# Kernel tuning notes

Measured on AMD Instinct MI355X. Metric: run time of the kernel, lower is better.

Reference implementation:

```python
import jax, jax.numpy as jnp
import numpy as np

N_EMBED = 1024
N_HEAD = 64  # head (value) dimension, per source: Linear(n_embed, n_head)
B = 8
C = 2048


def setup_inputs() -> dict:
    key = jax.random.key(0)
    k1, k2, k3, k4, k5 = jax.random.split(key, 5)
    bound = 1.0 / np.sqrt(N_EMBED)  # torch Linear default init range
    x = jax.random.normal(k1, (B, C, N_EMBED), dtype=jnp.float32)
    Wq = jax.random.uniform(k2, (N_EMBED, N_HEAD), dtype=jnp.float32, minval=-bound, maxval=bound)
    Wk = jax.random.uniform(k3, (N_EMBED, N_HEAD), dtype=jnp.float32, minval=-bound, maxval=bound)
    Wv = jax.random.uniform(k4, (N_EMBED, N_HEAD), dtype=jnp.float32, minval=-bound, maxval=bound)
    zero_mask = jax.random.randint(k5, (B, C), 0, 2) == 1
    return {"x": x, "Wq": Wq, "Wk": Wk, "Wv": Wv, "zero_mask": zero_mask}


def reference(x, Wq, Wk, Wv, zero_mask):
    # x: [B, C, n_embed]; zero_mask: [B, C] bool (zeroes whole query rows post-softmax)
    Bc, Cc, _ = x.shape
    q = x @ Wq  # [B, C, H]
    k = x @ Wk
    v = x @ Wv
    # NOTE: source scales by C**-0.5 (sequence length), not head_dim**-0.5
    scores = jnp.einsum('bqh,bkh->bqk', q, k) * (float(Cc) ** -0.5)  # [B, C, C]
    causal = jnp.tril(jnp.ones((Cc, Cc), dtype=bool))
    scores = jnp.where(causal[None], scores, -jnp.inf)
    a = jax.nn.softmax(scores, axis=-1)
    a = jnp.where(zero_mask[..., None], jnp.zeros((), dtype=a.dtype), a)  # post-softmax zero mask
    return a @ v  # [B, C, H]
```

## Files before the change

### kernel.cpp

```cpp
#include <hip/hip_runtime.h>
#include <math.h>


#define B_ 8
#define C_ 2048
#define E_ 1024
#define H_ 64
#define SCALE 0.02209708691207961f

typedef __attribute__((ext_vector_type(8))) short short8;
typedef __attribute__((ext_vector_type(4))) float floatx4;

union BF8 { short8 s8; unsigned int u[4]; };

static __device__ __forceinline__ unsigned int pack_bf2(float lo, float hi) {
    unsigned int a = __builtin_bit_cast(unsigned int, lo);
    unsigned int b = __builtin_bit_cast(unsigned int, hi);
    return (a >> 16) | (b & 0xFFFF0000u);
}
static __device__ __forceinline__ unsigned short f2bf(float f) {
    return (unsigned short)(__builtin_bit_cast(unsigned int, f) >> 16);
}
static __device__ __forceinline__ void load_lds16(const void* g, void* l) {
    __builtin_amdgcn_global_load_lds(
        (const __attribute__((address_space(1))) void*)g,
        (__attribute__((address_space(3))) void*)l, 16, 0, 0);
}

__global__ __launch_bounds__(256) void wcvt_kernel(
    const float* __restrict__ Wq, const float* __restrict__ Wk,
    const float* __restrict__ Wv, unsigned short* __restrict__ wt)
{
    __shared__ float lds[64][68];
    const int bid = (int)blockIdx.x;
    const int m = bid >> 4, kt = bid & 15, k0 = kt * 64;
    const float* W = (m == 0) ? Wq : (m == 1) ? Wk : Wv;
    const int t = (int)threadIdx.x;
#pragma unroll
    for (int j = 0; j < 4; j++) {
        int idx4 = j * 256 + t;
        int row = idx4 >> 4, c4 = idx4 & 15;
        float4 v = *(const float4*)(W + (size_t)(k0 + row) * 64 + c4 * 4);
        *(float4*)&lds[row][c4 * 4] = v;
    }
    __syncthreads();
#pragma unroll
    for (int j = 0; j < 2; j++) {
        int g = j * 256 + t;
        int n = g >> 3, kk = (g & 7) * 8;
        unsigned int o[4];
#pragma unroll
        for (int i = 0; i < 4; i++)
            o[i] = pack_bf2(lds[kk + 2 * i][n], lds[kk + 2 * i + 1][n]);
        *(uint4*)(wt + (size_t)(m * 64 + n) * 1024 + k0 + kk) =
            make_uint4(o[0], o[1], o[2], o[3]);
    }
}

__global__ __launch_bounds__(256, 2) void qkv_kernel(
    const float* __restrict__ X, const unsigned short* __restrict__ wt,
    unsigned short* __restrict__ qg, unsigned short* __restrict__ kg,
    unsigned short* __restrict__ vtile)
{
    __shared__ unsigned short wlds[2][192 * 64];
    __shared__ unsigned short vstage[64 * 40];

    const int t = (int)threadIdx.x;
    const int w = t >> 6, lane = t & 63;
    const int l15 = lane & 15, quad = lane >> 4;
    const int r0 = (int)blockIdx.x * 32;
    const int mrow = r0 + (w >> 1) * 16 + l15;
    const int ncol0 = (w & 1) * 96;

    const int srow_off = lane >> 3;
    const int sgs = lane & 7;

    floatx4 acc[6];
#pragma unroll
    for (int j = 0; j < 6; j++) acc[j] = (floatx4){0.f, 0.f, 0.f, 0.f};

#pragma unroll
    for (int j = 0; j < 6; j++) {
        const int region = w * 6 + j;
        const int row = region * 8 + srow_off;
        const int gsrc = sgs ^ (row & 7);
        load_lds16(wt + (size_t)row * 1024 + gsrc * 8, &wlds[0][region * 512]);
    }
    float4 xr[4];
#pragma unroll
    for (int kc = 0; kc < 2; kc++) {
        const float* xp = X + (size_t)mrow * E_ + kc * 32 + quad * 8;
        xr[kc * 2]     = *(const float4*)xp;
        xr[kc * 2 + 1] = *(const float4*)(xp + 4);
    }

    int buf = 0;
    for (int c = 0; c < 16; c++) {
        __syncthreads();
        float4 xr2[4];
        if (c < 15) {
            const int k0n = (c + 1) * 64;
#pragma unroll
            for (int kc = 0; kc < 2; kc++) {
                const float* xp = X + (size_t)mrow * E_ + k0n + kc * 32 + quad * 8;
                xr2[kc * 2]     = *(const float4*)xp;
                xr2[kc * 2 + 1] = *(const float4*)(xp + 4);
            }
#pragma unroll
            for (int j = 0; j < 6; j++) {
                const int region = w * 6 + j;
                const int row = region * 8 + srow_off;
                const int gsrc = sgs ^ (row & 7);
                load_lds16(wt + (size_t)row * 1024 + k0n + gsrc * 8,
                           &wlds[buf ^ 1][region * 512]);
            }
        }
#pragma unroll
        for (int kc = 0; kc < 2; kc++) {
            BF8 a;
            float4 f0 = xr[kc * 2], f1 = xr[kc * 2 + 1];
            a.u[0] = pack_bf2(f0.x, f0.y);
            a.u[1] = pack_bf2(f0.z, f0.w);
            a.u[2] = pack_bf2(f1.x, f1.y);
            a.u[3] = pack_bf2(f1.z, f1.w);
#pragma unroll
            for (int nt = 0; nt < 6; nt++) {
                const int n = ncol0 + nt * 16 + l15;
                const int g = kc * 4 + quad;
                short8 bfr = *(const short8*)&wlds[buf][n * 64 + (g ^ (n & 7)) * 8];
                acc[nt] = __builtin_amdgcn_mfma_f32_16x16x32_bf16(
                    a.s8, bfr, acc[nt], 0, 0, 0);
            }
        }
#pragma unroll
        for (int j = 0; j < 4; j++) xr[j] = xr2[j];
        buf ^= 1;
    }

    const int bb = r0 >> 11;
    const int keybase = r0 & 2047;
    const int rowl0 = (w >> 1) * 16 + quad * 4;
#pragma unroll
    for (int nt = 0; nt < 6; nt++) {
        const int n = ncol0 + nt * 16 + l15;
        if (n < 64) {
#pragma unroll
            for (int r = 0; r < 4; r++)
                qg[(size_t)(r0 + rowl0 + r) * 64 + n] = f2bf(acc[nt][r] * SCALE);
        } else if (n < 128) {
#pragma unroll
            for (int r = 0; r < 4; r++)
                kg[(size_t)(r0 + rowl0 + r) * 64 + (n - 64)] = f2bf(acc[nt][r]);
        } else {
            const int h = n - 128;
            unsigned int p0 = pack_bf2(acc[nt][0], acc[nt][1]);
            unsigned int p1 = pack_bf2(acc[nt][2], acc[nt][3]);
            *(unsigned int*)&vstage[h * 40 + rowl0] = p0;
            *(unsigned int*)&vstage[h * 40 + rowl0 + 2] = p1;
        }
    }
    __syncthreads();
    {
        const int h = t >> 2, part = t & 3;
        uint4 v = *(const uint4*)&vstage[h * 40 + part * 8];
        *(uint4*)(vtile + ((size_t)(bb * 32 + (keybase >> 6)) * 64 + h) * 64
                  + (keybase & 63) + part * 8) = v;
    }
}

__global__ __launch_bounds__(128, 2) void attn_kernel(
    const unsigned short* __restrict__ qg, const unsigned short* __restrict__ kg,
    const unsigned short* __restrict__ vtile, const int* __restrict__ zmask,
    float* __restrict__ opart, float* __restrict__ lpart,
    float* __restrict__ out)
{
    __shared__ unsigned short Klds[2][64 * 64];
    __shared__ unsigned short Vlds[2][64 * 64];
    __shared__ unsigned short Ps[2 * 16 * 88];

    const int t = (int)threadIdx.x;
    const int w = t >> 6, lane = t & 63;
    const int l15 = lane & 15, quad = lane >> 4;
    const int b = (int)blockIdx.x;
    const int qt = (int)blockIdx.y;
    const int z = (int)blockIdx.z;
    const int q0 = qt * 32;
    const int nkt = (q0 >> 6) + 1;
    const int t0 = z * 16;
    const int t1 = (z == 0) ? ((nkt < 16) ? nkt : 16) : nkt;
    if (t0 >= t1) return;

    const int qlo = q0 + w * 16;
    const int myrow = qlo + quad * 4;
    const int srow_off = lane >> 3, sgs = lane & 7;

    short8 qfr[2];
#pragma unroll
    for (int kc = 0; kc < 2; kc++)
        qfr[kc] = *(const short8*)(qg + ((size_t)b * C_ + qlo + l15) * 64
                                   + kc * 32 + quad * 8);

    floatx4 accO[4];
#pragma unroll
    for (int i = 0; i < 4; i++) accO[i] = (floatx4){0.f, 0.f, 0.f, 0.f};
    float lsum[4] = {0.f, 0.f, 0.f, 0.f};

#pragma unroll
    for (int j = 0; j < 4; j++) {
        const int region = w * 4 + j;
        const int row = region * 8 + srow_off;
        const int gsrc = sgs ^ (row & 7);
        load_lds16(kg + ((size_t)b * C_ + t0 * 64 + row) * 64 + gsrc * 8,
                   &Klds[0][region * 512]);
        load_lds16(vtile + (((size_t)b * 32 + t0) * 64 + row) * 64 + gsrc * 8,
                   &Vlds[0][region * 512]);
    }

    int buf = 0;
    for (int kt = t0; kt < t1; kt++) {
        __syncthreads();
        if (kt + 1 < t1) {
            const int k0n = (kt + 1) * 64;
#pragma unroll
            for (int j = 0; j < 4; j++) {
                const int region = w * 4 + j;
                const int row = region * 8 + srow_off;
                const int gsrc = sgs ^ (row & 7);
                load_lds16(kg + ((size_t)b * C_ + k0n + row) * 64 + gsrc * 8,
                           &Klds[buf ^ 1][region * 512]);
                load_lds16(vtile + (((size_t)b * 32 + kt + 1) * 64 + row) * 64 + gsrc * 8,
                           &Vlds[buf ^ 1][region * 512]);
            }
        }

        floatx4 s[4];
#pragma unroll
        for (int nt = 0; nt < 4; nt++) {
            const int row = nt * 16 + l15;
            short8 kf0 = *(const short8*)&Klds[buf][row * 64 + ((quad) ^ (row & 7)) * 8];
            short8 kf1 = *(const short8*)&Klds[buf][row * 64 + ((4 + quad) ^ (row & 7)) * 8];
            floatx4 zz = (floatx4){0.f, 0.f, 0.f, 0.f};
            zz = __builtin_amdgcn_mfma_f32_16x16x32_bf16(qfr[0], kf0, zz, 0, 0, 0);
            s[nt] = __builtin_amdgcn_mfma_f32_16x16x32_bf16(qfr[1], kf1, zz, 0, 0, 0);
        }
        float pr[4][4];
#pragma unroll
        for (int nt = 0; nt < 4; nt++)
#pragma unroll
            for (int r = 0; r < 4; r++) pr[nt][r] = __expf(s[nt][r]);
        if (kt == nkt - 1) {
            const int k0 = kt * 64;
#pragma unroll
            for (int nt = 0; nt < 4; nt++) {
                const int key = k0 + nt * 16 + l15;
#pragma unroll
                for (int r = 0; r < 4; r++)
                    if (key > myrow + r) pr[nt][r] = 0.f;
            }
        }
#pragma unroll
        for (int nt = 0; nt < 4; nt++)
#pragma unroll
            for (int r = 0; r < 4; r++) {
                lsum[r] += pr[nt][r];
                Ps[(w * 16 + quad * 4 + r) * 88 + nt * 16 + l15] = f2bf(pr[nt][r]);
            }
#pragma unroll
        for (int kc = 0; kc < 2; kc++) {
            short8 af = *(const short8*)&Ps[(w * 16 + l15) * 88 + kc * 32 + quad * 8];
#pragma unroll
            for (int nt = 0; nt < 4; nt++) {
                const int row = nt * 16 + l15;
                short8 vf = *(const short8*)&Vlds[buf][row * 64
                                + ((kc * 4 + quad) ^ (row & 7)) * 8];
                accO[nt] = __builtin_amdgcn_mfma_f32_16x16x32_bf16(
                    af, vf, accO[nt], 0, 0, 0);
            }
        }
        buf ^= 1;
    }

#pragma unroll
    for (int r = 0; r < 4; r++) {
        float v = lsum[r];
        v += __shfl_xor(v, 1);
        v += __shfl_xor(v, 2);
        v += __shfl_xor(v, 4);
        v += __shfl_xor(v, 8);
        lsum[r] = v;
    }

    if (q0 < 1024) {
        float inv[4];
#pragma unroll
        for (int r = 0; r < 4; r++) {
            int zm = zmask[b * C_ + myrow + r];
            inv[r] = zm ? 0.f : 1.0f / lsum[r];
        }
#pragma unroll
        for (int nt = 0; nt < 4; nt++)
#pragma unroll
            for (int r = 0; r < 4; r++)
                out[(size_t)(b * C_ + myrow + r) * 64 + nt * 16 + l15] =
                    accO[nt][r] * inv[r];
    } else {
        const int lrow = myrow - 1024;
        float* ob = opart + ((size_t)(z * 8 + b) * 1024 + lrow) * 64;
#pragma unroll
        for (int nt = 0; nt < 4; nt++)
#pragma unroll
            for (int r = 0; r < 4; r++)
                ob[(size_t)r * 64 + nt * 16 + l15] = accO[nt][r];
        if (l15 == 0) {
#pragma unroll
            for (int r = 0; r < 4; r++)
                lpart[(size_t)(z * 8 + b) * 1024 + lrow + r] = lsum[r];
        }
    }
}

__global__ __launch_bounds__(256) void combine_kernel(
    const float* __restrict__ opart, const float* __restrict__ lpart,
    const int* __restrict__ zmask, float* __restrict__ out)
{
    const int gid = (int)blockIdx.x * 256 + (int)threadIdx.x;
    const int b = gid >> 14;
    const int rem = gid & 16383;
    const int lrow = rem >> 4;
    const int f4 = rem & 15;

    const size_t o0 = ((size_t)(0 * 8 + b) * 1024 + lrow) * 64 + f4 * 4;
    const size_t o1 = ((size_t)(1 * 8 + b) * 1024 + lrow) * 64 + f4 * 4;
    float4 a = *(const float4*)(opart + o0);
    float4 c = *(const float4*)(opart + o1);
    float l = lpart[(size_t)(0 * 8 + b) * 1024 + lrow]
            + lpart[(size_t)(1 * 8 + b) * 1024 + lrow];
    const int row = 1024 + lrow;
    const float inv = zmask[b * C_ + row] ? 0.f : 1.0f / l;
    *(float4*)(out + (size_t)(b * C_ + row) * 64 + f4 * 4) =
        make_float4((a.x + c.x) * inv, (a.y + c.y) * inv,
                    (a.z + c.z) * inv, (a.w + c.w) * inv);
}

extern "C" void kernel_launch(void* const* d_in, const int* in_sizes, int n_in,
                              void* d_out, int out_size, void* d_ws, size_t ws_size,
                              hipStream_t stream) {
    const float* X  = (const float*)d_in[0];
    const float* Wq = (const float*)d_in[1];
    const float* Wk = (const float*)d_in[2];
    const float* Wv = (const float*)d_in[3];
    const int*   zm = (const int*)d_in[4];
    float* out = (float*)d_out;

    unsigned short* qg    = (unsigned short*)d_ws;
    unsigned short* kg    = qg    + (size_t)B_ * C_ * H_;
    unsigned short* vtile = kg    + (size_t)B_ * C_ * H_;
    unsigned short* wt    = vtile + (size_t)B_ * C_ * H_;
    float* opart = (float*)(wt + (size_t)192 * 1024);
    float* lpart = opart + (size_t)2 * 8 * 1024 * 64;

    wcvt_kernel<<<dim3(48), dim3(256), 0, stream>>>(Wq, Wk, Wv, wt);
    qkv_kernel<<<dim3(512), dim3(256), 0, stream>>>(X, wt, qg, kg, vtile);
    attn_kernel<<<dim3(B_, 64, 2), dim3(128), 0, stream>>>(
        qg, kg, vtile, zm, opart, lpart, out);
    combine_kernel<<<dim3(512), dim3(256), 0, stream>>>(opart, lpart, zm, out);
}
```

Measured before the change: 148.0 us.

## Drop LDS staging and shrink attention blocks to single-wave with finer KV split

```diff
diff --git a/kernel.cpp b/kernel.cpp
--- a/kernel.cpp
+++ b/kernel.cpp
@@ -20,11 +20,6 @@
 }
 static __device__ __forceinline__ unsigned short f2bf(float f) {
     return (unsigned short)(__builtin_bit_cast(unsigned int, f) >> 16);
-}
-static __device__ __forceinline__ void load_lds16(const void* g, void* l) {
-    __builtin_amdgcn_global_load_lds(
-        (const __attribute__((address_space(1))) void*)g,
-        (__attribute__((address_space(3))) void*)l, 16, 0, 0);
 }
 
 __global__ __launch_bounds__(256) void wcvt_kernel(
@@ -57,12 +52,11 @@
     }
 }
 
-__global__ __launch_bounds__(256, 2) void qkv_kernel(
+__global__ __launch_bounds__(256, 4) void qkv_kernel(
     const float* __restrict__ X, const unsigned short* __restrict__ wt,
     unsigned short* __restrict__ qg, unsigned short* __restrict__ kg,
     unsigned short* __restrict__ vtile)
 {
-    __shared__ unsigned short wlds[2][192 * 64];
     __shared__ unsigned short vstage[64 * 40];
 
     const int t = (int)threadIdx.x;
@@ -72,20 +66,10 @@
     const int mrow = r0 + (w >> 1) * 16 + l15;
     const int ncol0 = (w & 1) * 96;
 
-    const int srow_off = lane >> 3;
-    const int sgs = lane & 7;
-
     floatx4 acc[6];
 #pragma unroll
     for (int j = 0; j < 6; j++) acc[j] = (floatx4){0.f, 0.f, 0.f, 0.f};
 
-#pragma unroll
-    for (int j = 0; j < 6; j++) {
-        const int region = w * 6 + j;
-        const int row = region * 8 + srow_off;
-        const int gsrc = sgs ^ (row & 7);
-        load_lds16(wt + (size_t)row * 1024 + gsrc * 8, &wlds[0][region * 512]);
-    }
     float4 xr[4];
 #pragma unroll
     for (int kc = 0; kc < 2; kc++) {
@@ -94,25 +78,25 @@
         xr[kc * 2 + 1] = *(const float4*)(xp + 4);
     }
 
-    int buf = 0;
     for (int c = 0; c < 16; c++) {
-        __syncthreads();
+        const int k0 = c * 64;
+        short8 bfr[2][6];
+#pragma unroll
+        for (int kc = 0; kc < 2; kc++)
+#pragma unroll
+            for (int nt = 0; nt < 6; nt++) {
+                const int n = ncol0 + nt * 16 + l15;
+                bfr[kc][nt] = *(const short8*)(wt + (size_t)n * 1024 + k0
+                                              + kc * 32 + quad * 8);
+            }
         float4 xr2[4];
         if (c < 15) {
-            const int k0n = (c + 1) * 64;
+            const int k0n = k0 + 64;
 #pragma unroll
             for (int kc = 0; kc < 2; kc++) {
                 const float* xp = X + (size_t)mrow * E_ + k0n + kc * 32 + quad * 8;
                 xr2[kc * 2]     = *(const float4*)xp;
                 xr2[kc * 2 + 1] = *(const float4*)(xp + 4);
-            }
-#pragma unroll
-            for (int j = 0; j < 6; j++) {
-                const int region = w * 6 + j;
-                const int row = region * 8 + srow_off;
-                const int gsrc = sgs ^ (row & 7);
-                load_lds16(wt + (size_t)row * 1024 + k0n + gsrc * 8,
-                           &wlds[buf ^ 1][region * 512]);
             }
         }
 #pragma unroll
@@ -124,17 +108,12 @@
             a.u[2] = pack_bf2(f1.x, f1.y);
             a.u[3] = pack_bf2(f1.z, f1.w);
 #pragma unroll
-            for (int nt = 0; nt < 6; nt++) {
-                const int n = ncol0 + nt * 16 + l15;
-                const int g = kc * 4 + quad;
-                short8 bfr = *(const short8*)&wlds[buf][n * 64 + (g ^ (n & 7)) * 8];
+            for (int nt = 0; nt < 6; nt++)
                 acc[nt] = __builtin_amdgcn_mfma_f32_16x16x32_bf16(
-                    a.s8, bfr, acc[nt], 0, 0, 0);
-            }
+                    a.s8, bfr[kc][nt], acc[nt], 0, 0, 0);
         }
 #pragma unroll
         for (int j = 0; j < 4; j++) xr[j] = xr2[j];
-        buf ^= 1;
     }
 
     const int bb = r0 >> 11;
@@ -168,36 +147,31 @@
     }
 }
 
-__global__ __launch_bounds__(128, 2) void attn_kernel(
+__global__ __launch_bounds__(64, 4) void attn_kernel(
     const unsigned short* __restrict__ qg, const unsigned short* __restrict__ kg,
     const unsigned short* __restrict__ vtile, const int* __restrict__ zmask,
     float* __restrict__ opart, float* __restrict__ lpart,
     float* __restrict__ out)
 {
-    __shared__ unsigned short Klds[2][64 * 64];
-    __shared__ unsigned short Vlds[2][64 * 64];
-    __shared__ unsigned short Ps[2 * 16 * 88];
-
-    const int t = (int)threadIdx.x;
-    const int w = t >> 6, lane = t & 63;
+    __shared__ unsigned short Ps[16 * 88];
+
+    const int lane = (int)threadIdx.x;
     const int l15 = lane & 15, quad = lane >> 4;
     const int b = (int)blockIdx.x;
     const int qt = (int)blockIdx.y;
     const int z = (int)blockIdx.z;
-    const int q0 = qt * 32;
-    const int nkt = (q0 >> 6) + 1;
-    const int t0 = z * 16;
-    const int t1 = (z == 0) ? ((nkt < 16) ? nkt : 16) : nkt;
+    const int q0 = qt * 16;
+    const int nkt = (qt >> 2) + 1;
+    const int t0 = z * 8;
+    const int t1 = (t0 + 8 < nkt) ? (t0 + 8) : nkt;
     if (t0 >= t1) return;
-
-    const int qlo = q0 + w * 16;
-    const int myrow = qlo + quad * 4;
-    const int srow_off = lane >> 3, sgs = lane & 7;
+    const int ns = (nkt + 7) >> 3;
+    const int myrow = q0 + quad * 4;
 
     short8 qfr[2];
 #pragma unroll
     for (int kc = 0; kc < 2; kc++)
-        qfr[kc] = *(const short8*)(qg + ((size_t)b * C_ + qlo + l15) * 64
+        qfr[kc] = *(const short8*)(qg + ((size_t)b * C_ + q0 + l15) * 64
                                    + kc * 32 + quad * 8);
 
     floatx4 accO[4];
@@ -205,43 +179,31 @@
     for (int i = 0; i < 4; i++) accO[i] = (floatx4){0.f, 0.f, 0.f, 0.f};
     float lsum[4] = {0.f, 0.f, 0.f, 0.f};
 
-#pragma unroll
-    for (int j = 0; j < 4; j++) {
-        const int region = w * 4 + j;
-        const int row = region * 8 + srow_off;
-        const int gsrc = sgs ^ (row & 7);
-        load_lds16(kg + ((size_t)b * C_ + t0 * 64 + row) * 64 + gsrc * 8,
-                   &Klds[0][region * 512]);
-        load_lds16(vtile + (((size_t)b * 32 + t0) * 64 + row) * 64 + gsrc * 8,
-                   &Vlds[0][region * 512]);
-    }
-
-    int buf = 0;
     for (int kt = t0; kt < t1; kt++) {
-        __syncthreads();
-        if (kt + 1 < t1) {
-            const int k0n = (kt + 1) * 64;
-#pragma unroll
-            for (int j = 0; j < 4; j++) {
-                const int region = w * 4 + j;
-                const int row = region * 8 + srow_off;
-                const int gsrc = sgs ^ (row & 7);
-                load_lds16(kg + ((size_t)b * C_ + k0n + row) * 64 + gsrc * 8,
-                           &Klds[buf ^ 1][region * 512]);
-                load_lds16(vtile + (((size_t)b * 32 + kt + 1) * 64 + row) * 64 + gsrc * 8,
-                           &Vlds[buf ^ 1][region * 512]);
-            }
-        }
+        const int k0 = kt * 64;
+        short8 kf[4][2];
+#pragma unroll
+        for (int nt = 0; nt < 4; nt++)
+#pragma unroll
+            for (int kc = 0; kc < 2; kc++)
+                kf[nt][kc] = *(const short8*)(kg
+                    + ((size_t)b * C_ + k0 + nt * 16 + l15) * 64
+                    + kc * 32 + quad * 8);
+        short8 vf[4][2];
+#pragma unroll
+        for (int nt = 0; nt < 4; nt++)
+#pragma unroll
+            for (int kc = 0; kc < 2; kc++)
+                vf[nt][kc] = *(const short8*)(vtile
+                    + (((size_t)b * 32 + kt) * 64 + nt * 16 + l15) * 64
+                    + kc * 32 + quad * 8);
 
         floatx4 s[4];
 #pragma unroll
         for (int nt = 0; nt < 4; nt++) {
-            const int row = nt * 16 + l15;
-            short8 kf0 = *(const short8*)&Klds[buf][row * 64 + ((quad) ^ (row & 7)) * 8];
-            short8 kf1 = *(const short8*)&Klds[buf][row * 64 + ((4 + quad) ^ (row & 7)) * 8];
             floatx4 zz = (floatx4){0.f, 0.f, 0.f, 0.f};
-            zz = __builtin_amdgcn_mfma_f32_16x16x32_bf16(qfr[0], kf0, zz, 0, 0, 0);
-            s[nt] = __builtin_amdgcn_mfma_f32_16x16x32_bf16(qfr[1], kf1, zz, 0, 0, 0);
+            zz = __builtin_amdgcn_mfma_f32_16x16x32_bf16(qfr[0], kf[nt][0], zz, 0, 0, 0);
+            s[nt] = __builtin_amdgcn_mfma_f32_16x16x32_bf16(qfr[1], kf[nt][1], zz, 0, 0, 0);
         }
         float pr[4][4];
 #pragma unroll
@@ -249,7 +211,6 @@
 #pragma unroll
             for (int r = 0; r < 4; r++) pr[nt][r] = __expf(s[nt][r]);
         if (kt == nkt - 1) {
-            const int k0 = kt * 64;
 #pragma unroll
             for (int nt = 0; nt < 4; nt++) {
                 const int key = k0 + nt * 16 + l15;
@@ -263,21 +224,16 @@
 #pragma unroll
             for (int r = 0; r < 4; r++) {
                 lsum[r] += pr[nt][r];
-                Ps[(w * 16 + quad * 4 + r) * 88 + nt * 16 + l15] = f2bf(pr[nt][r]);
+                Ps[(quad * 4 + r) * 88 + nt * 16 + l15] = f2bf(pr[nt][r]);
             }
 #pragma unroll
         for (int kc = 0; kc < 2; kc++) {
-            short8 af = *(const short8*)&Ps[(w * 16 + l15) * 88 + kc * 32 + quad * 8];
-#pragma unroll
-            for (int nt = 0; nt < 4; nt++) {
-                const int row = nt * 16 + l15;
-                short8 vf = *(const short8*)&Vlds[buf][row * 64
-                                + ((kc * 4 + quad) ^ (row & 7)) * 8];
+            short8 af = *(const short8*)&Ps[l15 * 88 + kc * 32 + quad * 8];
+#pragma unroll
+            for (int nt = 0; nt < 4; nt++)
                 accO[nt] = __builtin_amdgcn_mfma_f32_16x16x32_bf16(
-                    af, vf, accO[nt], 0, 0, 0);
-            }
-        }
-        buf ^= 1;
+                    af, vf[nt][kc], accO[nt], 0, 0, 0);
+        }
     }
 
 #pragma unroll
@@ -290,7 +246,7 @@
         lsum[r] = v;
     }
 
-    if (q0 < 1024) {
+    if (ns == 1) {
         float inv[4];
 #pragma unroll
         for (int r = 0; r < 4; r++) {
@@ -304,8 +260,8 @@
                 out[(size_t)(b * C_ + myrow + r) * 64 + nt * 16 + l15] =
                     accO[nt][r] * inv[r];
     } else {
-        const int lrow = myrow - 1024;
-        float* ob = opart + ((size_t)(z * 8 + b) * 1024 + lrow) * 64;
+        const int lrow = myrow - 512;
+        float* ob = opart + ((size_t)(z * 8 + b) * 1536 + lrow) * 64;
 #pragma unroll
         for (int nt = 0; nt < 4; nt++)
 #pragma unroll
@@ -314,7 +270,7 @@
         if (l15 == 0) {
 #pragma unroll
             for (int r = 0; r < 4; r++)
-                lpart[(size_t)(z * 8 + b) * 1024 + lrow + r] = lsum[r];
+                lpart[(size_t)(z * 8 + b) * 1536 + lrow + r] = lsum[r];
         }
     }
 }
@@ -323,23 +279,25 @@
     const float* __restrict__ opart, const float* __restrict__ lpart,
     const int* __restrict__ zmask, float* __restrict__ out)
 {
+    const int b = (int)blockIdx.y;
     const int gid = (int)blockIdx.x * 256 + (int)threadIdx.x;
-    const int b = gid >> 14;
-    const int rem = gid & 16383;
-    const int lrow = rem >> 4;
-    const int f4 = rem & 15;
-
-    const size_t o0 = ((size_t)(0 * 8 + b) * 1024 + lrow) * 64 + f4 * 4;
-    const size_t o1 = ((size_t)(1 * 8 + b) * 1024 + lrow) * 64 + f4 * 4;
-    float4 a = *(const float4*)(opart + o0);
-    float4 c = *(const float4*)(opart + o1);
-    float l = lpart[(size_t)(0 * 8 + b) * 1024 + lrow]
-            + lpart[(size_t)(1 * 8 + b) * 1024 + lrow];
-    const int row = 1024 + lrow;
+    const int lrow = gid >> 4;
+    const int f4 = gid & 15;
+    const int row = 512 + lrow;
+    const int nkt = (row >> 6) + 1;
+    const int ns = (nkt + 7) >> 3;
+
+    float4 o = make_float4(0.f, 0.f, 0.f, 0.f);
+    float l = 0.f;
+    for (int zc = 0; zc < ns; zc++) {
+        float4 p = *(const float4*)(opart
+            + ((size_t)(zc * 8 + b) * 1536 + lrow) * 64 + f4 * 4);
+        o.x += p.x; o.y += p.y; o.z += p.z; o.w += p.w;
+        l += lpart[(size_t)(zc * 8 + b) * 1536 + lrow];
+    }
     const float inv = zmask[b * C_ + row] ? 0.f : 1.0f / l;
     *(float4*)(out + (size_t)(b * C_ + row) * 64 + f4 * 4) =
-        make_float4((a.x + c.x) * inv, (a.y + c.y) * inv,
-                    (a.z + c.z) * inv, (a.w + c.w) * inv);
+        make_float4(o.x * inv, o.y * inv, o.z * inv, o.w * inv);
 }
 
 extern "C" void kernel_launch(void* const* d_in, const int* in_sizes, int n_in,
@@ -357,11 +315,11 @@
     unsigned short* vtile = kg    + (size_t)B_ * C_ * H_;
     unsigned short* wt    = vtile + (size_t)B_ * C_ * H_;
     float* opart = (float*)(wt + (size_t)192 * 1024);
-    float* lpart = opart + (size_t)2 * 8 * 1024 * 64;
+    float* lpart = opart + (size_t)4 * 8 * 1536 * 64;
 
     wcvt_kernel<<<dim3(48), dim3(256), 0, stream>>>(Wq, Wk, Wv, wt);
     qkv_kernel<<<dim3(512), dim3(256), 0, stream>>>(X, wt, qg, kg, vtile);
-    attn_kernel<<<dim3(B_, 64, 2), dim3(128), 0, stream>>>(
+    attn_kernel<<<dim3(B_, 128, 4), dim3(64), 0, stream>>>(
         qg, kg, vtile, zm, opart, lpart, out);
-    combine_kernel<<<dim3(512), dim3(256), 0, stream>>>(opart, lpart, zm, out);
-}
+    combine_kernel<<<dim3(96, B_), dim3(256), 0, stream>>>(opart, lpart, zm, out);
+}
```

Result: slower. 198.0 us (+33.8%).
